# Optimization experiments

Measured on AMD Instinct MI355X. Metric: run time of the kernel, lower is better.

The kernel has to match this reference:

```python
import jax, jax.numpy as jnp
import numpy as np

EPS = 1e-8

def setup_inputs() -> dict:
    key = jax.random.key(0)
    k1, k2, k3, k4 = jax.random.split(key, 4)
    x_cnn = jax.random.normal(k1, (8, 256, 128, 128), dtype=jnp.float32)
    x_vit = jax.random.normal(k2, (8, 512, 32, 32), dtype=jnp.float32)
    W = jax.random.normal(k3, (256, 512), dtype=jnp.float32) * 0.05  # 1x1 conv weight
    b = jax.random.normal(k4, (256,), dtype=jnp.float32) * 0.05
    return {"x_cnn": x_cnn, "x_vit": x_vit, "W": W, "b": b}

def reference(x_cnn, x_vit, W, b):
    # 1x1 conv projection: 512 -> cnn_channels
    v = jnp.einsum('oc,bchw->bohw', W, x_vit) + b[None, :, None, None]
    B, C, H, Wd = x_cnn.shape
    if v.shape[2:] != (H, Wd):
        # bilinear, half-pixel centers == torch align_corners=False
        v = jax.image.resize(v, (B, C, H, Wd), method='bilinear')
    # Per-pixel cosine similarity over channels. The original computes a full
    # (HW x HW) bmm and keeps only the diagonal; the diagonal equals this
    # per-pixel channel dot product, so the math is identical.
    dot = jnp.sum(x_cnn * v, axis=1)               # [B,H,W]
    n_cnn = jnp.sqrt(jnp.sum(x_cnn * x_cnn, axis=1))
    n_vit = jnp.sqrt(jnp.sum(v * v, axis=1))
    sim = dot / (n_cnn * n_vit + EPS)
    return sim[:, None, :, :]                      # [B,1,H,W]
```

## Files before the change

### kernel.cpp

```cpp
#include <hip/hip_runtime.h>
#include <hip/hip_bf16.h>

typedef __attribute__((ext_vector_type(8))) short bf16x8;
typedef __attribute__((ext_vector_type(4))) float f32x4;
typedef __attribute__((ext_vector_type(8))) unsigned short u16x8;

static __device__ __forceinline__ unsigned short f2bf(float f) {
    union { float f; unsigned int u; } v; v.f = f;
    unsigned int u = v.u;
    u += 0x7FFFu + ((u >> 16) & 1u);
    return (unsigned short)(u >> 16);
}

__global__ void __launch_bounds__(256) prep(const float* __restrict__ X,
                                            unsigned short* __restrict__ Xt,
                                            const float* __restrict__ W,
                                            unsigned short* __restrict__ Wbf) {
    __shared__ unsigned short ls[64][65];
    int blk = blockIdx.x;
    int t   = threadIdx.x;

    if (blk >= 1024) {
        int i = ((blk - 1024) * 256 + t) * 4;
        float4 v = *(const float4*)(W + i);
        ushort4 o;
        o.x = f2bf(v.x); o.y = f2bf(v.y); o.z = f2bf(v.z); o.w = f2bf(v.w);
        *(ushort4*)(Wbf + i) = o;
        return;
    }

    int b  = blk >> 7;
    int c0 = ((blk >> 4) & 7) * 64;
    int p0 = (blk & 15) * 64;

    const float* src = X + ((size_t)b * 512 + c0) * 1024 + p0;
    int cc = t >> 4;
    int p4 = (t & 15) << 2;
    #pragma unroll
    for (int i = 0; i < 4; ++i) {
        int c = cc + i * 16;
        float4 v = *(const float4*)(src + (size_t)c * 1024 + p4);
        ls[p4 + 0][c] = f2bf(v.x);
        ls[p4 + 1][c] = f2bf(v.y);
        ls[p4 + 2][c] = f2bf(v.z);
        ls[p4 + 3][c] = f2bf(v.w);
    }
    __syncthreads();

    unsigned short* dst = Xt + ((size_t)b * 1024 + p0) * 512 + c0;
    int pp  = t >> 2;
    int c16 = (t & 3) << 4;
    u16x8 w0, w1;
    #pragma unroll
    for (int j = 0; j < 8; ++j) { w0[j] = ls[pp][c16 + j]; w1[j] = ls[pp][c16 + 8 + j]; }
    *(u16x8*)(dst + (size_t)pp * 512 + c16)     = w0;
    *(u16x8*)(dst + (size_t)pp * 512 + c16 + 8) = w1;
}

__global__ void __launch_bounds__(256) gemm_bf16(const unsigned short* __restrict__ Wbf,
                                                 const unsigned short* __restrict__ Xt,
                                                 const float* __restrict__ bias,
                                                 float* __restrict__ V) {
    __shared__ __align__(16) unsigned short As[2][4 * 64 * 8];
    __shared__ __align__(16) unsigned short Bs[2][4 * 64 * 8];

    int b  = blockIdx.z;
    int m0 = blockIdx.y * 64;
    int n0 = blockIdx.x * 64;
    int t  = threadIdx.x;
    int wave = t >> 6;
    int lane = t & 63;
    int wm = (wave >> 1) * 32;
    int wn = (wave & 1) * 32;
    int l15  = lane & 15;
    int quad = lane >> 4;

    int koct = t & 3;
    int mrow = t >> 2;

    const unsigned short* Aglob = Wbf + (size_t)(m0 + mrow) * 512 + (koct << 3);
    const unsigned short* Bglob = Xt + ((size_t)b * 1024 + n0 + mrow) * 512 + (koct << 3);
    int stIdx = (koct * 512 + mrow * 8) ^ (koct * 8);

    int ia0 = (quad * 512 + (wm      + l15) * 8) ^ (quad * 8);
    int ia1 = (quad * 512 + (wm + 16 + l15) * 8) ^ (quad * 8);
    int ib0 = (quad * 512 + (wn      + l15) * 8) ^ (quad * 8);
    int ib1 = (quad * 512 + (wn + 16 + l15) * 8) ^ (quad * 8);

    f32x4 acc[2][2] = {};

    u16x8 ra = *(const u16x8*)(Aglob);
    u16x8 rb = *(const u16x8*)(Bglob);
    *(u16x8*)(As[0] + stIdx) = ra;
    *(u16x8*)(Bs[0] + stIdx) = rb;
    __syncthreads();

    for (int k0 = 0; k0 < 512; k0 += 32) {
        int p = (k0 >> 5) & 1;
        bool more = (k0 + 32) < 512;
        if (more) {
            ra = *(const u16x8*)(Aglob + k0 + 32);
            rb = *(const u16x8*)(Bglob + k0 + 32);
        }

        bf16x8 a0 = *(const bf16x8*)(As[p] + ia0);
        bf16x8 a1 = *(const bf16x8*)(As[p] + ia1);
        bf16x8 b0 = *(const bf16x8*)(Bs[p] + ib0);
        bf16x8 b1 = *(const bf16x8*)(Bs[p] + ib1);

        acc[0][0] = __builtin_amdgcn_mfma_f32_16x16x32_bf16(a0, b0, acc[0][0], 0, 0, 0);
        acc[0][1] = __builtin_amdgcn_mfma_f32_16x16x32_bf16(a0, b1, acc[0][1], 0, 0, 0);
        acc[1][0] = __builtin_amdgcn_mfma_f32_16x16x32_bf16(a1, b0, acc[1][0], 0, 0, 0);
        acc[1][1] = __builtin_amdgcn_mfma_f32_16x16x32_bf16(a1, b1, acc[1][1], 0, 0, 0);

        if (more) {
            *(u16x8*)(As[p ^ 1] + stIdx) = ra;
            *(u16x8*)(Bs[p ^ 1] + stIdx) = rb;
        }
        __syncthreads();
    }

    #pragma unroll
    for (int mi = 0; mi < 2; ++mi)
        #pragma unroll
        for (int ni = 0; ni < 2; ++ni)
            #pragma unroll
            for (int r = 0; r < 4; ++r) {
                int gm = m0 + wm + mi * 16 + quad * 4 + r;
                int gn = n0 + wn + ni * 16 + l15;
                V[((size_t)b * 256 + gm) * 1024 + gn] = acc[mi][ni][r] + bias[gm];
            }
}

__global__ void __launch_bounds__(256) fused_cos(const float* __restrict__ xcnn,
                                                 const float* __restrict__ V,
                                                 float* __restrict__ out) {
    __shared__ float sh[9216];

    int bh = blockIdx.x;
    int b  = bh >> 7;
    int h  = bh & 127;
    int t  = threadIdx.x;
    int q  = t & 31;
    int cs = t >> 5;

    float sy = (h + 0.5f) * 0.25f - 0.5f;
    float fy = floorf(sy);
    float dy = sy - fy;
    int y0 = max(0, min(31, (int)fy));
    int y1 = max(0, min(31, (int)fy + 1));
    float ry = dy, ry0 = 1.f - dy;

    {
        int ch8 = t >> 3;
        int c4  = (t & 7) << 2;
        #pragma unroll
        for (int p = 0; p < 8; ++p) {
            int ch = p * 32 + ch8;
            const float* vr = V + ((size_t)(b * 256 + ch) * 1024);
            float4 top = *(const float4*)(vr + y0 * 32 + c4);
            float4 bot = *(const float4*)(vr + y1 * 32 + c4);
            float4 bl;
            bl.x = ry0 * top.x + ry * bot.x;
            bl.y = ry0 * top.y + ry * bot.y;
            bl.z = ry0 * top.z + ry * bot.z;
            bl.w = ry0 * top.w + ry * bot.w;
            *(float4*)&sh[ch * 36 + c4] = bl;
        }
    }
    __syncthreads();

    int cb = max(0, min(28, q - 1));
    float a[4][4];
    #pragma unroll
    for (int px = 0; px < 4; ++px) {
        #pragma unroll
        for (int j = 0; j < 4; ++j) a[px][j] = 0.f;
        int w = q * 4 + px;
        float sx = (w + 0.5f) * 0.25f - 0.5f;
        float fx = floorf(sx);
        float dx = sx - fx;
        int x0 = max(0, min(31, (int)fx));
        int x1 = max(0, min(31, (int)fx + 1));
        a[px][x0 - cb] += 1.f - dx;
        a[px][x1 - cb] += dx;
    }

    const float* xp = xcnn + ((size_t)(b * 256 + cs * 32) * 16384) + h * 128 + q * 4;

    float dot[4] = {0.f, 0.f, 0.f, 0.f};
    float nx [4] = {0.f, 0.f, 0.f, 0.f};
    float nv [4] = {0.f, 0.f, 0.f, 0.f};

    #pragma unroll 8
    for (int c = 0; c < 32; ++c) {
        float4 xv = *(const float4*)(xp + (size_t)c * 16384);
        const float* vl = sh + (cs * 32 + c) * 36 + cb;
        float v0 = vl[0], v1 = vl[1], v2 = vl[2], v3 = vl[3];
        float xs[4] = {xv.x, xv.y, xv.z, xv.w};
        #pragma unroll
        for (int px = 0; px < 4; ++px) {
            float v = a[px][0] * v0 + a[px][1] * v1 + a[px][2] * v2 + a[px][3] * v3;
            dot[px] += xs[px] * v;
            nx [px] += xs[px] * xs[px];
            nv [px] += v * v;
        }
    }

    __syncthreads();
    float* my = sh + cs * 385;
    #pragma unroll
    for (int px = 0; px < 4; ++px) {
        int o = (q * 4 + px) * 3;
        my[o + 0] = dot[px];
        my[o + 1] = nx[px];
        my[o + 2] = nv[px];
    }
    __syncthreads();

    if (t < 128) {
        int px = t & 3;
        int q2 = t >> 2;
        int o  = (q2 * 4 + px) * 3;
        float d = 0.f, sx2 = 0.f, sv2 = 0.f;
        #pragma unroll
        for (int s = 0; s < 8; ++s) {
            d   += sh[s * 385 + o + 0];
            sx2 += sh[s * 385 + o + 1];
            sv2 += sh[s * 385 + o + 2];
        }
        out[(size_t)b * 16384 + h * 128 + q2 * 4 + px] =
            d / (sqrtf(sx2) * sqrtf(sv2) + 1e-8f);
    }
}

extern "C" void kernel_launch(void* const* d_in, const int* in_sizes, int n_in,
                              void* d_out, int out_size, void* d_ws, size_t ws_size,
                              hipStream_t stream) {
    const float* x_cnn = (const float*)d_in[0];
    const float* x_vit = (const float*)d_in[1];
    const float* W     = (const float*)d_in[2];
    const float* bias  = (const float*)d_in[3];
    float* out = (float*)d_out;

    char* ws = (char*)d_ws;
    float*          V   = (float*)ws;
    unsigned short* Xt  = (unsigned short*)(ws + 8388608);
    unsigned short* Wbf = (unsigned short*)(ws + 16777216);

    prep<<<1152, 256, 0, stream>>>(x_vit, Xt, W, Wbf);
    gemm_bf16<<<dim3(16, 4, 8), 256, 0, stream>>>(Wbf, Xt, bias, V);
    fused_cos<<<1024, 256, 0, stream>>>(x_cnn, V, out);
}
```

Before: 223.2 us.

## Fuse bf16 conversion and transpose of W and x_vit into GEMM loads

Removes the separate prep kernel that converted W and x_vit to bf16 and transposed x_vit to pixel-major layout. The GEMM now reads fp32 directly, converting to bf16 in registers and loading B column-strided (8 channel rows per thread, coalesced across pixels) into the same swizzled LDS layout. This drops one kernel launch and an intermediate write and read of the bf16 activations. In exchange, every M-block re-reads and re-converts the fp32 activations, and the scalar strided loads replace vector loads.

```diff
diff --git a/kernel.cpp b/kernel.cpp
--- a/kernel.cpp
+++ b/kernel.cpp
@@ -12,55 +12,10 @@
     return (unsigned short)(u >> 16);
 }
 
-__global__ void __launch_bounds__(256) prep(const float* __restrict__ X,
-                                            unsigned short* __restrict__ Xt,
-                                            const float* __restrict__ W,
-                                            unsigned short* __restrict__ Wbf) {
-    __shared__ unsigned short ls[64][65];
-    int blk = blockIdx.x;
-    int t   = threadIdx.x;
-
-    if (blk >= 1024) {
-        int i = ((blk - 1024) * 256 + t) * 4;
-        float4 v = *(const float4*)(W + i);
-        ushort4 o;
-        o.x = f2bf(v.x); o.y = f2bf(v.y); o.z = f2bf(v.z); o.w = f2bf(v.w);
-        *(ushort4*)(Wbf + i) = o;
-        return;
-    }
-
-    int b  = blk >> 7;
-    int c0 = ((blk >> 4) & 7) * 64;
-    int p0 = (blk & 15) * 64;
-
-    const float* src = X + ((size_t)b * 512 + c0) * 1024 + p0;
-    int cc = t >> 4;
-    int p4 = (t & 15) << 2;
-    #pragma unroll
-    for (int i = 0; i < 4; ++i) {
-        int c = cc + i * 16;
-        float4 v = *(const float4*)(src + (size_t)c * 1024 + p4);
-        ls[p4 + 0][c] = f2bf(v.x);
-        ls[p4 + 1][c] = f2bf(v.y);
-        ls[p4 + 2][c] = f2bf(v.z);
-        ls[p4 + 3][c] = f2bf(v.w);
-    }
-    __syncthreads();
-
-    unsigned short* dst = Xt + ((size_t)b * 1024 + p0) * 512 + c0;
-    int pp  = t >> 2;
-    int c16 = (t & 3) << 4;
-    u16x8 w0, w1;
-    #pragma unroll
-    for (int j = 0; j < 8; ++j) { w0[j] = ls[pp][c16 + j]; w1[j] = ls[pp][c16 + 8 + j]; }
-    *(u16x8*)(dst + (size_t)pp * 512 + c16)     = w0;
-    *(u16x8*)(dst + (size_t)pp * 512 + c16 + 8) = w1;
-}
-
-__global__ void __launch_bounds__(256) gemm_bf16(const unsigned short* __restrict__ Wbf,
-                                                 const unsigned short* __restrict__ Xt,
-                                                 const float* __restrict__ bias,
-                                                 float* __restrict__ V) {
+__global__ void __launch_bounds__(256) gemm_fused(const float* __restrict__ W,
+                                                  const float* __restrict__ Xv,
+                                                  const float* __restrict__ bias,
+                                                  float* __restrict__ V) {
     __shared__ __align__(16) unsigned short As[2][4 * 64 * 8];
     __shared__ __align__(16) unsigned short Bs[2][4 * 64 * 8];
 
@@ -75,12 +30,15 @@
     int l15  = lane & 15;
     int quad = lane >> 4;
 
-    int koct = t & 3;
-    int mrow = t >> 2;
-
-    const unsigned short* Aglob = Wbf + (size_t)(m0 + mrow) * 512 + (koct << 3);
-    const unsigned short* Bglob = Xt + ((size_t)b * 1024 + n0 + mrow) * 512 + (koct << 3);
-    int stIdx = (koct * 512 + mrow * 8) ^ (koct * 8);
+    int ka = t & 3;
+    int ma = t >> 2;
+    const float* Ag = W + (size_t)(m0 + ma) * 512 + (ka << 3);
+    int stA = (ka * 512 + ma * 8) ^ (ka * 8);
+
+    int kb = t >> 6;
+    int nb = t & 63;
+    const float* Bg = Xv + ((size_t)b * 512 + (kb << 3)) * 1024 + n0 + nb;
+    int stB = (kb * 512 + nb * 8) ^ (kb * 8);
 
     int ia0 = (quad * 512 + (wm      + l15) * 8) ^ (quad * 8);
     int ia1 = (quad * 512 + (wm + 16 + l15) * 8) ^ (quad * 8);
@@ -89,18 +47,33 @@
 
     f32x4 acc[2][2] = {};
 
-    u16x8 ra = *(const u16x8*)(Aglob);
-    u16x8 rb = *(const u16x8*)(Bglob);
-    *(u16x8*)(As[0] + stIdx) = ra;
-    *(u16x8*)(Bs[0] + stIdx) = rb;
+    u16x8 ra, rb;
+    {
+        float4 x = *(const float4*)(Ag);
+        float4 y = *(const float4*)(Ag + 4);
+        ra[0] = (short)f2bf(x.x); ra[1] = (short)f2bf(x.y);
+        ra[2] = (short)f2bf(x.z); ra[3] = (short)f2bf(x.w);
+        ra[4] = (short)f2bf(y.x); ra[5] = (short)f2bf(y.y);
+        ra[6] = (short)f2bf(y.z); ra[7] = (short)f2bf(y.w);
+        #pragma unroll
+        for (int j = 0; j < 8; ++j) rb[j] = (short)f2bf(Bg[(size_t)j * 1024]);
+    }
+    *(u16x8*)(As[0] + stA) = ra;
+    *(u16x8*)(Bs[0] + stB) = rb;
     __syncthreads();
 
     for (int k0 = 0; k0 < 512; k0 += 32) {
         int p = (k0 >> 5) & 1;
         bool more = (k0 + 32) < 512;
         if (more) {
-            ra = *(const u16x8*)(Aglob + k0 + 32);
-            rb = *(const u16x8*)(Bglob + k0 + 32);
+            float4 x = *(const float4*)(Ag + k0 + 32);
+            float4 y = *(const float4*)(Ag + k0 + 36);
+            ra[0] = (short)f2bf(x.x); ra[1] = (short)f2bf(x.y);
+            ra[2] = (short)f2bf(x.z); ra[3] = (short)f2bf(x.w);
+            ra[4] = (short)f2bf(y.x); ra[5] = (short)f2bf(y.y);
+            ra[6] = (short)f2bf(y.z); ra[7] = (short)f2bf(y.w);
+            #pragma unroll
+            for (int j = 0; j < 8; ++j) rb[j] = (short)f2bf(Bg[(size_t)(k0 + 32 + j) * 1024]);
         }
 
         bf16x8 a0 = *(const bf16x8*)(As[p] + ia0);
@@ -114,8 +87,8 @@
         acc[1][1] = __builtin_amdgcn_mfma_f32_16x16x32_bf16(a1, b1, acc[1][1], 0, 0, 0);
 
         if (more) {
-            *(u16x8*)(As[p ^ 1] + stIdx) = ra;
-            *(u16x8*)(Bs[p ^ 1] + stIdx) = rb;
+            *(u16x8*)(As[p ^ 1] + stA) = ra;
+            *(u16x8*)(Bs[p ^ 1] + stB) = rb;
         }
         __syncthreads();
     }
@@ -243,12 +216,8 @@
     const float* bias  = (const float*)d_in[3];
     float* out = (float*)d_out;
 
-    char* ws = (char*)d_ws;
-    float*          V   = (float*)ws;
-    unsigned short* Xt  = (unsigned short*)(ws + 8388608);
-    unsigned short* Wbf = (unsigned short*)(ws + 16777216);
-
-    prep<<<1152, 256, 0, stream>>>(x_vit, Xt, W, Wbf);
-    gemm_bf16<<<dim3(16, 4, 8), 256, 0, stream>>>(Wbf, Xt, bias, V);
+    float* V = (float*)d_ws;
+
+    gemm_fused<<<dim3(16, 4, 8), 256, 0, stream>>>(W, x_vit, bias, V);
     fused_cos<<<1024, 256, 0, stream>>>(x_cnn, V, out);
 }
```

After: 229.6 us. +2.9%, slower.
